# Performance work log

Hardware: AMD Instinct MI355X
Metric: run time of the kernel (lower is better)

Reference implementation:

```python
import jax, jax.numpy as jnp
import numpy as np

PI = np.pi


def _apply_1q(state, gate, wire, n):
    # state: [B, 2**n] complex64; gate: [2,2] (shared) or [B,2,2] (per-sample)
    # PennyLane convention: wire 0 is the most-significant bit of the state index.
    B = state.shape[0]
    left, right = 2 ** wire, 2 ** (n - wire - 1)
    s = state.reshape(B, left, 2, right)
    if gate.ndim == 2:
        s = jnp.einsum('kl,balr->bakr', gate, s)
    else:
        s = jnp.einsum('bkl,balr->bakr', gate, s)
    return s.reshape(B, -1)


def _apply_cz(state, wire, n):
    # CZ on (wire, wire+1): flip sign of |..11..> amplitudes
    B = state.shape[0]
    left, right = 2 ** wire, 2 ** (n - wire - 2)
    s = state.reshape(B, left, 2, 2, right)
    s = s.at[:, :, 1, 1, :].multiply(-1.0)
    return s.reshape(B, -1)


def _ry_batched(theta):
    # theta: [B] -> [B,2,2] complex RY(theta)
    h = 0.5 * theta
    c, s = jnp.cos(h), jnp.sin(h)
    g = jnp.stack([jnp.stack([c, -s], -1), jnp.stack([s, c], -1)], -2)
    return g.astype(jnp.complex64)


def _rot(phi, theta, omega):
    # Rot = RZ(omega) @ RY(theta) @ RZ(phi)
    c, s = jnp.cos(0.5 * theta), jnp.sin(0.5 * theta)
    e_mm = jnp.exp(-0.5j * (phi + omega))
    e_pm = jnp.exp(0.5j * (phi - omega))
    e_mp = jnp.exp(-0.5j * (phi - omega))
    e_pp = jnp.exp(0.5j * (phi + omega))
    g = jnp.stack([jnp.stack([e_mm * c, -e_pm * s]), jnp.stack([e_mp * s, e_pp * c])])
    return g.astype(jnp.complex64)


def _simulate(enc, weights):
    # enc: [B, n_qubits] in [-1,1]; weights: [n_layers, n_qubits, 3]
    n_layers, n, _ = weights.shape
    B = enc.shape[0]
    state = jnp.zeros((B, 2 ** n), jnp.complex64).at[:, 0].set(1.0)
    ry = [_ry_batched(enc[:, i] * PI) for i in range(n)]
    for l in range(n_layers):
        for i in range(n):
            state = _apply_1q(state, ry[i], i, n)
        for i in range(n):
            state = _apply_1q(state, _rot(weights[l, i, 0], weights[l, i, 1], weights[l, i, 2]), i, n)
        for i in range(n - 1):
            state = _apply_cz(state, i, n)
    for i in range(n):
        state = _apply_1q(state, ry[i], i, n)
    probs = state.real ** 2 + state.imag ** 2  # [B, 2**n]
    # <Z_i> = sum_k probs[k] * (-1)^bit_i(k), wire 0 = MSB
    bits = (jnp.arange(2 ** n)[None, :] >> (n - 1 - jnp.arange(n))[:, None]) & 1
    signs = (1 - 2 * bits).astype(probs.dtype)  # [n, 2**n]
    return probs @ signs.T  # [B, n]


def setup_inputs() -> dict:
    B, D, NQ, NL, NA = 32768, 16, 8, 4, 4
    key = jax.random.key(0)
    ks = jax.random.split(key, 6)

    def lin(k, o, i):
        b = 1.0 / np.sqrt(i)
        k1, k2 = jax.random.split(k)
        return (jax.random.uniform(k1, (o, i), jnp.float32, -b, b),
                jax.random.uniform(k2, (o,), jnp.float32, -b, b))

    enc_w1, enc_b1 = lin(ks[1], 8, D)
    enc_w2, enc_b2 = lin(ks[2], NQ, 8)
    dec_w1, dec_b1 = lin(ks[3], 8, NQ)
    dec_w2, dec_b2 = lin(ks[4], NA, 8)
    q_weights = jax.random.uniform(ks[5], (NL, NQ, 3), jnp.float32, 0.0, 2.0 * PI)
    x = jax.random.normal(ks[0], (B, D), jnp.float32)
    return {"x": x, "enc_w1": enc_w1, "enc_b1": enc_b1, "enc_w2": enc_w2, "enc_b2": enc_b2,
            "q_weights": q_weights, "dec_w1": dec_w1, "dec_b1": dec_b1, "dec_w2": dec_w2, "dec_b2": dec_b2}


def reference(x, enc_w1, enc_b1, enc_w2, enc_b2, q_weights, dec_w1, dec_b1, dec_w2, dec_b2):
    h = jax.nn.relu(x @ enc_w1.T + enc_b1)
    enc = jnp.tanh(h @ enc_w2.T + enc_b2)          # [B, n_qubits]
    q = _simulate(enc, q_weights)                  # [B, n_qubits] PauliZ expvals
    h2 = jax.nn.relu(q @ dec_w1.T + dec_b1)
    return h2 @ dec_w2.T + dec_b2                  # [B, n_actions]
```

## Files before the change

kernel.cpp:

```cpp
#include <hip/hip_runtime.h>
#include <math.h>


#define PI_F 3.14159265358979323846f

typedef float v2f __attribute__((ext_vector_type(2)));

struct C2 { float re, im; };
__device__ __forceinline__ C2 cmul(C2 a, C2 b) {
    C2 r;
    r.re = fmaf(a.re, b.re, -a.im * b.im);
    r.im = fmaf(a.re, b.im,  a.im * b.re);
    return r;
}
__device__ __forceinline__ float fxor(float x, int m) {
    return __int_as_float(__float_as_int(x) ^ m);
}

__device__ __forceinline__ v2f pk_mul(v2f a, v2f b) {
    v2f d; asm("v_pk_mul_f32 %0, %1, %2" : "=v"(d) : "v"(a), "v"(b)); return d;
}
__device__ __forceinline__ v2f pk_mul_neg(v2f a, v2f b) {
    v2f d; asm("v_pk_mul_f32 %0, %1, %2 neg_lo:[1,0] neg_hi:[1,0]"
               : "=v"(d) : "v"(a), "v"(b)); return d;
}
__device__ __forceinline__ v2f pk_fma(v2f a, v2f b, v2f c) {
    v2f d; asm("v_pk_fma_f32 %0, %1, %2, %3" : "=v"(d) : "v"(a), "v"(b), "v"(c)); return d;
}
__device__ __forceinline__ v2f pk_fma_nn(v2f a, v2f b, v2f c) {
    v2f d; asm("v_pk_fma_f32 %0, %1, %2, %3 neg_lo:[1,0,0] neg_hi:[1,0,0]"
               : "=v"(d) : "v"(a), "v"(b), "v"(c)); return d;
}
__device__ __forceinline__ v2f pk_fma_swl(v2f a, v2f b, v2f c) {
    v2f d; asm("v_pk_fma_f32 %0, %1, %2, %3 op_sel:[0,1,0] op_sel_hi:[1,0,1] neg_lo:[1,0,0]"
               : "=v"(d) : "v"(a), "v"(b), "v"(c)); return d;
}
__device__ __forceinline__ v2f pk_fma_swh(v2f a, v2f b, v2f c) {
    v2f d; asm("v_pk_fma_f32 %0, %1, %2, %3 op_sel:[0,1,0] op_sel_hi:[1,0,1] neg_hi:[1,0,0]"
               : "=v"(d) : "v"(a), "v"(b), "v"(c)); return d;
}
__device__ __forceinline__ v2f cmulv(v2f z, C2 c) {
    v2f n = pk_mul((v2f){c.re, c.re}, z);
    return pk_fma_swl((v2f){c.im, c.im}, z, n);
}

template<int CTRL>
__device__ __forceinline__ float dppf(float x) {
    int xi = __float_as_int(x);
    int r = __builtin_amdgcn_update_dpp(xi, xi, CTRL, 0xF, 0xF, false);
    return __int_as_float(r);
}
template<int M>
__device__ __forceinline__ float lxor(float x) {
    if constexpr (M == 1)      return dppf<0xB1>(x);
    else if constexpr (M == 2) return dppf<0x4E>(x);
    else                       return dppf<0x128>(x);
}

__device__ __forceinline__ void load_G2(const float* __restrict__ c_lds, int g,
                                        float cc, float ss,
                                        float& ar, float& ai, float& br, float& bi) {
    const float4 c0 = *(const float4*)(c_lds + 4 * g);
    ar = fmaf(c0.x, cc, -c0.z * ss);
    ai = fmaf(c0.y, cc,  c0.w * ss);
    br = fmaf(c0.z, cc,  c0.x * ss);
    bi = fmaf(c0.w, cc, -c0.y * ss);
}

template<int M>
__device__ __forceinline__ void su2_cross(v2f cSr, v2f cSi, v2f cOr, v2f cOi,
                                          v2f z[32]) {
#pragma unroll
    for (int c = 0; c < 4; c++) {
        v2f p[8];
#pragma unroll
        for (int k = 0; k < 8; k++) {
            p[k].x = lxor<M>(z[c * 8 + k].x);
            p[k].y = lxor<M>(z[c * 8 + k].y);
        }
#pragma unroll
        for (int k = 0; k < 8; k++) {
            const int t = c * 8 + k;
            v2f n = pk_mul(cSr, z[t]);
            n = pk_fma_swl(cSi, z[t], n);
            n = pk_fma   (cOr, p[k], n);
            n = pk_fma_swl(cOi, p[k], n);
            z[t] = n;
        }
    }
}

template<int ST>
__device__ __forceinline__ void su2_inlane(v2f arr, v2f aii, v2f brr, v2f bii,
                                           v2f z[32]) {
#pragma unroll
    for (int t = 0; t < 32; t++) {
        if ((t & ST) == 0) {
            const int u = t + ST;
            v2f x = z[t], y = z[u];
            v2f nx = pk_mul(arr, x);
            nx = pk_fma_swl(aii, x, nx);
            nx = pk_fma_nn (brr, y, nx);
            nx = pk_fma_swl(bii, y, nx);
            v2f ny = pk_mul(brr, x);
            ny = pk_fma_swl(bii, x, ny);
            ny = pk_fma   (arr, y, ny);
            ny = pk_fma_swh(aii, y, ny);
            z[t] = nx; z[u] = ny;
        }
    }
}

template<int M>
__device__ __forceinline__ void ry_cross(v2f cc, v2f cO, v2f z[32]) {
#pragma unroll
    for (int c = 0; c < 4; c++) {
        v2f p[8];
#pragma unroll
        for (int k = 0; k < 8; k++) {
            p[k].x = lxor<M>(z[c * 8 + k].x);
            p[k].y = lxor<M>(z[c * 8 + k].y);
        }
#pragma unroll
        for (int k = 0; k < 8; k++) {
            const int t = c * 8 + k;
            z[t] = pk_fma(cO, p[k], pk_mul(cc, z[t]));
        }
    }
}
template<int ST>
__device__ __forceinline__ void ry_inlane(v2f cc, v2f ss, v2f z[32]) {
#pragma unroll
    for (int t = 0; t < 32; t++) {
        if ((t & ST) == 0) {
            const int u = t + ST;
            v2f x = z[t], y = z[u];
            z[t] = pk_fma_nn(ss, y, pk_mul(cc, x));
            z[u] = pk_fma   (cc, y, pk_mul(ss, x));
        }
    }
}

__host__ __device__ constexpr bool czt5(int t) {
    return ((((t >> 4) & (t >> 3)) ^ ((t >> 3) & (t >> 2)) ^
             ((t >> 2) & (t >> 1)) ^ ((t >> 1) & t)) & 1) != 0;
}

__global__ __launch_bounds__(128, 2) void qdqn_kernel(
    const float* __restrict__ x,
    const float* __restrict__ ew1, const float* __restrict__ eb1,
    const float* __restrict__ ew2, const float* __restrict__ eb2,
    const float* __restrict__ qw,
    const float* __restrict__ dw1, const float* __restrict__ db1,
    const float* __restrict__ dw2, const float* __restrict__ db2,
    float* __restrict__ out, int B, int NL) {
    __shared__ __align__(16) float c_lds[32 * 4];
    __shared__ __align__(16) float hx[2][8][8];
    __shared__ __align__(16) float csx[2][8][16];

    const int tid = threadIdx.x;
    const int wave = tid >> 6;
    const int lane = tid & 63;
    const int g = (lane & 3) | ((lane >> 1) & 4);
    const int grp = ((lane >> 2) & 1) | ((lane >> 3) & 6);
    int s = blockIdx.x * 16 + wave * 8 + grp;
    if (s >= B) s = B - 1;

    float xv[16];
    {
        const float4* xp = (const float4*)(x + s * 16);
#pragma unroll
        for (int i = 0; i < 4; i++) {
            float4 v = xp[i];
            xv[4*i] = v.x; xv[4*i+1] = v.y; xv[4*i+2] = v.z; xv[4*i+3] = v.w;
        }
    }

    const int n_gates = NL * 8;
    if (tid < n_gates) {
        const int gg = tid;
        float phi = qw[3 * gg + 0], th = qw[3 * gg + 1], om = qw[3 * gg + 2];
        float c = __cosf(0.5f * th), sv = __sinf(0.5f * th);
        float A = 0.5f * (phi + om), Bb = 0.5f * (phi - om);
        float* o = c_lds + 4 * gg;
        o[0] =  __cosf(A) * c;   o[1] = -__sinf(A) * c;
        o[2] =  __cosf(Bb) * sv; o[3] = -__sinf(Bb) * sv;
    }
    __syncthreads();

    float cq[8], sq[8];
    {
        float a = eb1[g];
#pragma unroll
        for (int i = 0; i < 16; i++) a = fmaf(ew1[g * 16 + i], xv[i], a);
        hx[wave][grp][g] = fmaxf(a, 0.0f);
        __builtin_amdgcn_wave_barrier();
        float4 h01 = *(const float4*)&hx[wave][grp][0];
        float4 h23 = *(const float4*)&hx[wave][grp][4];
        float b = eb2[g];
        b = fmaf(ew2[g*8+0], h01.x, b); b = fmaf(ew2[g*8+1], h01.y, b);
        b = fmaf(ew2[g*8+2], h01.z, b); b = fmaf(ew2[g*8+3], h01.w, b);
        b = fmaf(ew2[g*8+4], h23.x, b); b = fmaf(ew2[g*8+5], h23.y, b);
        b = fmaf(ew2[g*8+6], h23.z, b); b = fmaf(ew2[g*8+7], h23.w, b);
        float e = 1.0f - __fdividef(2.0f, __expf(2.0f * b) + 1.0f);
        float ang = e * (0.5f * PI_F);
        float2* cso = (float2*)&csx[wave][grp][2 * g];
        *cso = make_float2(__cosf(ang), __sinf(ang));
        __builtin_amdgcn_wave_barrier();
#pragma unroll
        for (int k = 0; k < 4; k++) {
            float4 v = *(const float4*)&csx[wave][grp][4 * k];
            cq[2*k] = v.x; sq[2*k] = v.y; cq[2*k+1] = v.z; sq[2*k+1] = v.w;
        }
    }

    int hiM[3], loM[3];
#pragma unroll
    for (int q = 0; q < 3; q++) {
        int hi = (g >> (2 - q)) & 1;
        hiM[q] = hi << 31;
        loM[q] = hiM[q] ^ 0x80000000;
    }

    const int g0b = g & 1, g1b = (g >> 1) & 1, g2b = (g >> 2) & 1;
    const float mLo = ((g2b & g1b) ^ (g1b & g0b)) ? -1.0f : 1.0f;
    const float mHi = g0b ? -mLo : mLo;
    const v2f mLo2 = (v2f){mLo, mLo}, mHi2 = (v2f){mHi, mHi};

    v2f z[32];
    {
        C2 P; P.re = 1.0f; P.im = 0.0f;
        C2 A[5], Bc[5];
#pragma unroll
        for (int q = 0; q < 8; q++) {
            float ar, ai, br, bi;
            load_G2(c_lds, q, cq[q], sq[q], ar, ai, br, bi);
            if (q < 3) {
                const bool hi = (g >> (2 - q)) & 1;
                C2 f; f.re = hi ? br : ar; f.im = hi ? bi : ai;
                P = cmul(P, f);
            } else {
                A[q-3].re = ar;  A[q-3].im = ai;
                Bc[q-3].re = br; Bc[q-3].im = bi;
            }
        }
        z[0] = (v2f){P.re, P.im};
#pragma unroll
        for (int w = 0; w < 5; w++) {
            const int n = 1 << w;
#pragma unroll
            for (int i = n - 1; i >= 0; i--) {
                v2f v = z[i];
                z[2*i+1] = cmulv(v, Bc[w]);
                z[2*i]   = cmulv(v, A[w]);
            }
        }
#pragma unroll
        for (int t = 0; t < 32; t++) {
            v2f m = (t < 16) ? mLo2 : mHi2;
            z[t] = czt5(t) ? pk_mul_neg(m, z[t]) : pk_mul(m, z[t]);
        }
    }

    for (int l = 1; l < NL; l++) {
        const int gb = l * 8;
        float ar, ai, br, bi;
        load_G2(c_lds, gb+0, cq[0], sq[0], ar, ai, br, bi);
        su2_cross<8>((v2f){ar,ar}, (v2f){fxor(ai,hiM[0]),fxor(ai,hiM[0])},
                     (v2f){fxor(br,loM[0]),fxor(br,loM[0])}, (v2f){bi,bi}, z);
        load_G2(c_lds, gb+1, cq[1], sq[1], ar, ai, br, bi);
        su2_cross<2>((v2f){ar,ar}, (v2f){fxor(ai,hiM[1]),fxor(ai,hiM[1])},
                     (v2f){fxor(br,loM[1]),fxor(br,loM[1])}, (v2f){bi,bi}, z);
        load_G2(c_lds, gb+2, cq[2], sq[2], ar, ai, br, bi);
        su2_cross<1>((v2f){ar,ar}, (v2f){fxor(ai,hiM[2]),fxor(ai,hiM[2])},
                     (v2f){fxor(br,loM[2]),fxor(br,loM[2])}, (v2f){bi,bi}, z);
        load_G2(c_lds, gb+3, cq[3], sq[3], ar, ai, br, bi);
        su2_inlane<16>((v2f){ar,ar}, (v2f){ai,ai}, (v2f){br,br}, (v2f){bi,bi}, z);
        load_G2(c_lds, gb+4, cq[4], sq[4], ar, ai, br, bi);
        su2_inlane<8>((v2f){ar,ar}, (v2f){ai,ai}, (v2f){br,br}, (v2f){bi,bi}, z);
        load_G2(c_lds, gb+5, cq[5], sq[5], ar, ai, br, bi);
        su2_inlane<4>((v2f){ar,ar}, (v2f){ai,ai}, (v2f){br,br}, (v2f){bi,bi}, z);
        load_G2(c_lds, gb+6, cq[6], sq[6], ar, ai, br, bi);
        su2_inlane<2>((v2f){ar,ar}, (v2f){ai,ai}, (v2f){br,br}, (v2f){bi,bi}, z);
        load_G2(c_lds, gb+7, cq[7], sq[7], ar, ai, br, bi);
        su2_inlane<1>((v2f){ar,ar}, (v2f){ai,ai}, (v2f){br,br}, (v2f){bi,bi}, z);
#pragma unroll
        for (int t = 0; t < 32; t++) {
            v2f m = (t < 16) ? mLo2 : mHi2;
            z[t] = czt5(t) ? pk_mul_neg(m, z[t]) : pk_mul(m, z[t]);
        }
    }

    {
        v2f cc, cO, ss;
        cc=(v2f){cq[0],cq[0]}; cO=(v2f){fxor(sq[0],loM[0]),fxor(sq[0],loM[0])};
        ry_cross<8>(cc, cO, z);
        cc=(v2f){cq[1],cq[1]}; cO=(v2f){fxor(sq[1],loM[1]),fxor(sq[1],loM[1])};
        ry_cross<2>(cc, cO, z);
        cc=(v2f){cq[2],cq[2]}; cO=(v2f){fxor(sq[2],loM[2]),fxor(sq[2],loM[2])};
        ry_cross<1>(cc, cO, z);
        cc=(v2f){cq[3],cq[3]}; ss=(v2f){sq[3],sq[3]}; ry_inlane<16>(cc, ss, z);
        cc=(v2f){cq[4],cq[4]}; ss=(v2f){sq[4],sq[4]}; ry_inlane<8>(cc, ss, z);
        cc=(v2f){cq[5],cq[5]}; ss=(v2f){sq[5],sq[5]}; ry_inlane<4>(cc, ss, z);
        cc=(v2f){cq[6],cq[6]}; ss=(v2f){sq[6],sq[6]}; ry_inlane<2>(cc, ss, z);
        cc=(v2f){cq[7],cq[7]}; ss=(v2f){sq[7],sq[7]}; ry_inlane<1>(cc, ss, z);
    }

    float p[32];
#pragma unroll
    for (int t = 0; t < 32; t++) p[t] = fmaf(z[t].x, z[t].x, z[t].y * z[t].y);

    float s16[16], zW[8];
    {
        float d = 0.0f;
#pragma unroll
        for (int i = 0; i < 16; i++) {
            s16[i] = p[2*i] + p[2*i+1];
            d += p[2*i] - p[2*i+1];
        }
        zW[7] = d;
        float s8[8]; d = 0.0f;
#pragma unroll
        for (int i = 0; i < 8; i++) {
            s8[i] = s16[2*i] + s16[2*i+1];
            d += s16[2*i] - s16[2*i+1];
        }
        zW[6] = d;
        float s4[4]; d = 0.0f;
#pragma unroll
        for (int i = 0; i < 4; i++) {
            s4[i] = s8[2*i] + s8[2*i+1];
            d += s8[2*i] - s8[2*i+1];
        }
        zW[5] = d;
        float s2a = s4[0] + s4[1], s2b = s4[2] + s4[3];
        zW[4] = (s4[0] - s4[1]) + (s4[2] - s4[3]);
        float sumP = s2a + s2b;
        zW[3] = s2a - s2b;
        zW[0] = g2b ? -sumP : sumP;
        zW[1] = g1b ? -sumP : sumP;
        zW[2] = g0b ? -sumP : sumP;
    }
#pragma unroll
    for (int w = 0; w < 8; w++) zW[w] += lxor<1>(zW[w]);
#pragma unroll
    for (int w = 0; w < 8; w++) zW[w] += lxor<2>(zW[w]);
#pragma unroll
    for (int w = 0; w < 8; w++) zW[w] += lxor<8>(zW[w]);

    {
        float a = db1[g];
#pragma unroll
        for (int w = 0; w < 8; w++) a = fmaf(dw1[g * 8 + w], zW[w], a);
        hx[wave][grp][g] = fmaxf(a, 0.0f);
        __builtin_amdgcn_wave_barrier();
        float4 h01 = *(const float4*)&hx[wave][grp][0];
        float4 h23 = *(const float4*)&hx[wave][grp][4];
        const int o = g & 3;
        float acc = db2[o];
        acc = fmaf(dw2[o*8+0], h01.x, acc); acc = fmaf(dw2[o*8+1], h01.y, acc);
        acc = fmaf(dw2[o*8+2], h01.z, acc); acc = fmaf(dw2[o*8+3], h01.w, acc);
        acc = fmaf(dw2[o*8+4], h23.x, acc); acc = fmaf(dw2[o*8+5], h23.y, acc);
        acc = fmaf(dw2[o*8+6], h23.z, acc); acc = fmaf(dw2[o*8+7], h23.w, acc);
        out[s * 4 + o] = acc;
    }
}

extern "C" void kernel_launch(void* const* d_in, const int* in_sizes, int n_in,
                              void* d_out, int out_size, void* d_ws, size_t ws_size,
                              hipStream_t stream) {
    const float* x   = (const float*)d_in[0];
    const float* ew1 = (const float*)d_in[1];
    const float* eb1 = (const float*)d_in[2];
    const float* ew2 = (const float*)d_in[3];
    const float* eb2 = (const float*)d_in[4];
    const float* qw  = (const float*)d_in[5];
    const float* dw1 = (const float*)d_in[6];
    const float* db1 = (const float*)d_in[7];
    const float* dw2 = (const float*)d_in[8];
    const float* db2 = (const float*)d_in[9];
    float* out = (float*)d_out;

    int B = in_sizes[0] / 16;
    int n_gates = in_sizes[5] / 3;
    int NL = n_gates / 8;

    int blocks = (B + 15) / 16;
    qdqn_kernel<<<blocks, 128, 0, stream>>>(x, ew1, eb1, ew2, eb2, qw,
                                            dw1, db1, dw2, db2, out, B, NL);
}
```

Measured before the change: 116.4 us.

## Fold final RY layer into Z expectation via cross-correlation terms; use scalar-broadcast packed ops

The final layer of RY rotations is no longer applied to the state vector. Each <Z_w> is instead computed from the pre-rotation probabilities and a per-wire real cross term Re(conj(z_t) z_u), using cos(theta) and sin(theta) identities, which removes a full pass of 8 rotation gates over the state. Separately, the packed FMA/mul helpers now take scalar coefficients and broadcast them with op_sel_hi instead of building duplicated v2f pairs, which saves register moves and VGPRs. The risk lies in getting the sign and scale of the cross terms right, especially the factor of 2 versus 4 for cross-lane wires, and in how reliably the op_sel operand broadcast works.

```diff
diff --git a/kernel.cpp b/kernel.cpp
--- a/kernel.cpp
+++ b/kernel.cpp
@@ -17,31 +17,50 @@
     return __int_as_float(__float_as_int(x) ^ m);
 }
 
-__device__ __forceinline__ v2f pk_mul(v2f a, v2f b) {
-    v2f d; asm("v_pk_mul_f32 %0, %1, %2" : "=v"(d) : "v"(a), "v"(b)); return d;
-}
-__device__ __forceinline__ v2f pk_mul_neg(v2f a, v2f b) {
-    v2f d; asm("v_pk_mul_f32 %0, %1, %2 neg_lo:[1,0] neg_hi:[1,0]"
-               : "=v"(d) : "v"(a), "v"(b)); return d;
-}
 __device__ __forceinline__ v2f pk_fma(v2f a, v2f b, v2f c) {
     v2f d; asm("v_pk_fma_f32 %0, %1, %2, %3" : "=v"(d) : "v"(a), "v"(b), "v"(c)); return d;
 }
-__device__ __forceinline__ v2f pk_fma_nn(v2f a, v2f b, v2f c) {
-    v2f d; asm("v_pk_fma_f32 %0, %1, %2, %3 neg_lo:[1,0,0] neg_hi:[1,0,0]"
-               : "=v"(d) : "v"(a), "v"(b), "v"(c)); return d;
-}
-__device__ __forceinline__ v2f pk_fma_swl(v2f a, v2f b, v2f c) {
-    v2f d; asm("v_pk_fma_f32 %0, %1, %2, %3 op_sel:[0,1,0] op_sel_hi:[1,0,1] neg_lo:[1,0,0]"
-               : "=v"(d) : "v"(a), "v"(b), "v"(c)); return d;
-}
-__device__ __forceinline__ v2f pk_fma_swh(v2f a, v2f b, v2f c) {
-    v2f d; asm("v_pk_fma_f32 %0, %1, %2, %3 op_sel:[0,1,0] op_sel_hi:[1,0,1] neg_hi:[1,0,0]"
-               : "=v"(d) : "v"(a), "v"(b), "v"(c)); return d;
+
+__device__ __forceinline__ v2f mkbc(float c) { v2f r; r.x = c; return r; }
+
+__device__ __forceinline__ v2f pk_mul_s(float c, v2f z) {
+    v2f cb = mkbc(c), d;
+    asm("v_pk_mul_f32 %0, %1, %2 op_sel_hi:[0,1]"
+        : "=v"(d) : "v"(cb), "v"(z));
+    return d;
+}
+__device__ __forceinline__ v2f pk_mul_neg_s(float c, v2f z) {
+    v2f cb = mkbc(c), d;
+    asm("v_pk_mul_f32 %0, %1, %2 op_sel_hi:[0,1] neg_lo:[1,0] neg_hi:[1,0]"
+        : "=v"(d) : "v"(cb), "v"(z));
+    return d;
+}
+__device__ __forceinline__ v2f pk_fma_s(float c, v2f b, v2f acc) {
+    v2f cb = mkbc(c), d;
+    asm("v_pk_fma_f32 %0, %1, %2, %3 op_sel_hi:[0,1,1]"
+        : "=v"(d) : "v"(cb), "v"(b), "v"(acc));
+    return d;
+}
+__device__ __forceinline__ v2f pk_fma_nn_s(float c, v2f b, v2f acc) {
+    v2f cb = mkbc(c), d;
+    asm("v_pk_fma_f32 %0, %1, %2, %3 op_sel_hi:[0,1,1] neg_lo:[1,0,0] neg_hi:[1,0,0]"
+        : "=v"(d) : "v"(cb), "v"(b), "v"(acc));
+    return d;
+}
+__device__ __forceinline__ v2f pk_fma_swl_s(float c, v2f z, v2f acc) {
+    v2f cb = mkbc(c), d;
+    asm("v_pk_fma_f32 %0, %1, %2, %3 op_sel:[0,1,0] op_sel_hi:[0,0,1] neg_lo:[1,0,0]"
+        : "=v"(d) : "v"(cb), "v"(z), "v"(acc));
+    return d;
+}
+__device__ __forceinline__ v2f pk_fma_swh_s(float c, v2f z, v2f acc) {
+    v2f cb = mkbc(c), d;
+    asm("v_pk_fma_f32 %0, %1, %2, %3 op_sel:[0,1,0] op_sel_hi:[0,0,1] neg_hi:[1,0,0]"
+        : "=v"(d) : "v"(cb), "v"(z), "v"(acc));
+    return d;
 }
 __device__ __forceinline__ v2f cmulv(v2f z, C2 c) {
-    v2f n = pk_mul((v2f){c.re, c.re}, z);
-    return pk_fma_swl((v2f){c.im, c.im}, z, n);
+    return pk_fma_swl_s(c.im, z, pk_mul_s(c.re, z));
 }
 
 template<int CTRL>
@@ -68,7 +87,7 @@
 }
 
 template<int M>
-__device__ __forceinline__ void su2_cross(v2f cSr, v2f cSi, v2f cOr, v2f cOi,
+__device__ __forceinline__ void su2_cross(float cSr, float cSi, float cOr, float cOi,
                                           v2f z[32]) {
 #pragma unroll
     for (int c = 0; c < 4; c++) {
@@ -81,38 +100,39 @@
 #pragma unroll
         for (int k = 0; k < 8; k++) {
             const int t = c * 8 + k;
-            v2f n = pk_mul(cSr, z[t]);
-            n = pk_fma_swl(cSi, z[t], n);
-            n = pk_fma   (cOr, p[k], n);
-            n = pk_fma_swl(cOi, p[k], n);
+            v2f n = pk_mul_s(cSr, z[t]);
+            n = pk_fma_swl_s(cSi, z[t], n);
+            n = pk_fma_s    (cOr, p[k], n);
+            n = pk_fma_swl_s(cOi, p[k], n);
             z[t] = n;
         }
     }
 }
 
 template<int ST>
-__device__ __forceinline__ void su2_inlane(v2f arr, v2f aii, v2f brr, v2f bii,
+__device__ __forceinline__ void su2_inlane(float ar, float ai, float br, float bi,
                                            v2f z[32]) {
 #pragma unroll
     for (int t = 0; t < 32; t++) {
         if ((t & ST) == 0) {
             const int u = t + ST;
             v2f x = z[t], y = z[u];
-            v2f nx = pk_mul(arr, x);
-            nx = pk_fma_swl(aii, x, nx);
-            nx = pk_fma_nn (brr, y, nx);
-            nx = pk_fma_swl(bii, y, nx);
-            v2f ny = pk_mul(brr, x);
-            ny = pk_fma_swl(bii, x, ny);
-            ny = pk_fma   (arr, y, ny);
-            ny = pk_fma_swh(aii, y, ny);
+            v2f nx = pk_mul_s(ar, x);
+            nx = pk_fma_swl_s(ai, x, nx);
+            nx = pk_fma_nn_s (br, y, nx);
+            nx = pk_fma_swl_s(bi, y, nx);
+            v2f ny = pk_mul_s(br, x);
+            ny = pk_fma_swl_s(bi, x, ny);
+            ny = pk_fma_s    (ar, y, ny);
+            ny = pk_fma_swh_s(ai, y, ny);
             z[t] = nx; z[u] = ny;
         }
     }
 }
 
 template<int M>
-__device__ __forceinline__ void ry_cross(v2f cc, v2f cO, v2f z[32]) {
+__device__ __forceinline__ v2f xcorr_cross(const v2f z[32]) {
+    v2f acc = (v2f){0.0f, 0.0f};
 #pragma unroll
     for (int c = 0; c < 4; c++) {
         v2f p[8];
@@ -122,23 +142,17 @@
             p[k].y = lxor<M>(z[c * 8 + k].y);
         }
 #pragma unroll
-        for (int k = 0; k < 8; k++) {
-            const int t = c * 8 + k;
-            z[t] = pk_fma(cO, p[k], pk_mul(cc, z[t]));
-        }
-    }
+        for (int k = 0; k < 8; k++) acc = pk_fma(z[c * 8 + k], p[k], acc);
+    }
+    return acc;
 }
 template<int ST>
-__device__ __forceinline__ void ry_inlane(v2f cc, v2f ss, v2f z[32]) {
-#pragma unroll
-    for (int t = 0; t < 32; t++) {
-        if ((t & ST) == 0) {
-            const int u = t + ST;
-            v2f x = z[t], y = z[u];
-            z[t] = pk_fma_nn(ss, y, pk_mul(cc, x));
-            z[u] = pk_fma   (cc, y, pk_mul(ss, x));
-        }
-    }
+__device__ __forceinline__ v2f xcorr_inlane(const v2f z[32]) {
+    v2f acc = (v2f){0.0f, 0.0f};
+#pragma unroll
+    for (int t = 0; t < 32; t++)
+        if ((t & ST) == 0) acc = pk_fma(z[t], z[t + ST], acc);
+    return acc;
 }
 
 __host__ __device__ constexpr bool czt5(int t) {
@@ -225,7 +239,6 @@
     const int g0b = g & 1, g1b = (g >> 1) & 1, g2b = (g >> 2) & 1;
     const float mLo = ((g2b & g1b) ^ (g1b & g0b)) ? -1.0f : 1.0f;
     const float mHi = g0b ? -mLo : mLo;
-    const v2f mLo2 = (v2f){mLo, mLo}, mHi2 = (v2f){mHi, mHi};
 
     v2f z[32];
     {
@@ -257,8 +270,8 @@
         }
 #pragma unroll
         for (int t = 0; t < 32; t++) {
-            v2f m = (t < 16) ? mLo2 : mHi2;
-            z[t] = czt5(t) ? pk_mul_neg(m, z[t]) : pk_mul(m, z[t]);
+            const float m = (t < 16) ? mLo : mHi;
+            z[t] = czt5(t) ? pk_mul_neg_s(m, z[t]) : pk_mul_s(m, z[t]);
         }
     }
 
@@ -266,45 +279,37 @@
         const int gb = l * 8;
         float ar, ai, br, bi;
         load_G2(c_lds, gb+0, cq[0], sq[0], ar, ai, br, bi);
-        su2_cross<8>((v2f){ar,ar}, (v2f){fxor(ai,hiM[0]),fxor(ai,hiM[0])},
-                     (v2f){fxor(br,loM[0]),fxor(br,loM[0])}, (v2f){bi,bi}, z);
+        su2_cross<8>(ar, fxor(ai,hiM[0]), fxor(br,loM[0]), bi, z);
         load_G2(c_lds, gb+1, cq[1], sq[1], ar, ai, br, bi);
-        su2_cross<2>((v2f){ar,ar}, (v2f){fxor(ai,hiM[1]),fxor(ai,hiM[1])},
-                     (v2f){fxor(br,loM[1]),fxor(br,loM[1])}, (v2f){bi,bi}, z);
+        su2_cross<2>(ar, fxor(ai,hiM[1]), fxor(br,loM[1]), bi, z);
         load_G2(c_lds, gb+2, cq[2], sq[2], ar, ai, br, bi);
-        su2_cross<1>((v2f){ar,ar}, (v2f){fxor(ai,hiM[2]),fxor(ai,hiM[2])},
-                     (v2f){fxor(br,loM[2]),fxor(br,loM[2])}, (v2f){bi,bi}, z);
+        su2_cross<1>(ar, fxor(ai,hiM[2]), fxor(br,loM[2]), bi, z);
         load_G2(c_lds, gb+3, cq[3], sq[3], ar, ai, br, bi);
-        su2_inlane<16>((v2f){ar,ar}, (v2f){ai,ai}, (v2f){br,br}, (v2f){bi,bi}, z);
+        su2_inlane<16>(ar, ai, br, bi, z);
         load_G2(c_lds, gb+4, cq[4], sq[4], ar, ai, br, bi);
-        su2_inlane<8>((v2f){ar,ar}, (v2f){ai,ai}, (v2f){br,br}, (v2f){bi,bi}, z);
+        su2_inlane<8>(ar, ai, br, bi, z);
         load_G2(c_lds, gb+5, cq[5], sq[5], ar, ai, br, bi);
-        su2_inlane<4>((v2f){ar,ar}, (v2f){ai,ai}, (v2f){br,br}, (v2f){bi,bi}, z);
+        su2_inlane<4>(ar, ai, br, bi, z);
         load_G2(c_lds, gb+6, cq[6], sq[6], ar, ai, br, bi);
-        su2_inlane<2>((v2f){ar,ar}, (v2f){ai,ai}, (v2f){br,br}, (v2f){bi,bi}, z);
+        su2_inlane<2>(ar, ai, br, bi, z);
         load_G2(c_lds, gb+7, cq[7], sq[7], ar, ai, br, bi);
-        su2_inlane<1>((v2f){ar,ar}, (v2f){ai,ai}, (v2f){br,br}, (v2f){bi,bi}, z);
+        su2_inlane<1>(ar, ai, br, bi, z);
 #pragma unroll
         for (int t = 0; t < 32; t++) {
-            v2f m = (t < 16) ? mLo2 : mHi2;
-            z[t] = czt5(t) ? pk_mul_neg(m, z[t]) : pk_mul(m, z[t]);
-        }
-    }
-
-    {
-        v2f cc, cO, ss;
-        cc=(v2f){cq[0],cq[0]}; cO=(v2f){fxor(sq[0],loM[0]),fxor(sq[0],loM[0])};
-        ry_cross<8>(cc, cO, z);
-        cc=(v2f){cq[1],cq[1]}; cO=(v2f){fxor(sq[1],loM[1]),fxor(sq[1],loM[1])};
-        ry_cross<2>(cc, cO, z);
-        cc=(v2f){cq[2],cq[2]}; cO=(v2f){fxor(sq[2],loM[2]),fxor(sq[2],loM[2])};
-        ry_cross<1>(cc, cO, z);
-        cc=(v2f){cq[3],cq[3]}; ss=(v2f){sq[3],sq[3]}; ry_inlane<16>(cc, ss, z);
-        cc=(v2f){cq[4],cq[4]}; ss=(v2f){sq[4],sq[4]}; ry_inlane<8>(cc, ss, z);
-        cc=(v2f){cq[5],cq[5]}; ss=(v2f){sq[5],sq[5]}; ry_inlane<4>(cc, ss, z);
-        cc=(v2f){cq[6],cq[6]}; ss=(v2f){sq[6],sq[6]}; ry_inlane<2>(cc, ss, z);
-        cc=(v2f){cq[7],cq[7]}; ss=(v2f){sq[7],sq[7]}; ry_inlane<1>(cc, ss, z);
-    }
+            const float m = (t < 16) ? mLo : mHi;
+            z[t] = czt5(t) ? pk_mul_neg_s(m, z[t]) : pk_mul_s(m, z[t]);
+        }
+    }
+
+    v2f xa[8];
+    xa[0] = xcorr_cross<8>(z);
+    xa[1] = xcorr_cross<2>(z);
+    xa[2] = xcorr_cross<1>(z);
+    xa[3] = xcorr_inlane<16>(z);
+    xa[4] = xcorr_inlane<8>(z);
+    xa[5] = xcorr_inlane<4>(z);
+    xa[6] = xcorr_inlane<2>(z);
+    xa[7] = xcorr_inlane<1>(z);
 
     float p[32];
 #pragma unroll
@@ -341,6 +346,15 @@
         zW[1] = g1b ? -sumP : sumP;
         zW[2] = g0b ? -sumP : sumP;
     }
+
+#pragma unroll
+    for (int w = 0; w < 8; w++) {
+        const float c2 = fmaf(cq[w], cq[w], -sq[w] * sq[w]);
+        const float cs = cq[w] * sq[w];
+        const float s2 = (w < 3 ? 2.0f : 4.0f) * cs;
+        zW[w] = fmaf(c2, zW[w], -s2 * (xa[w].x + xa[w].y));
+    }
+
 #pragma unroll
     for (int w = 0; w < 8; w++) zW[w] += lxor<1>(zW[w]);
 #pragma unroll
```

Measured after the change: 116.8 us. Within noise of the previous version (+0.3%).
